# Optimization experiments

Measured on AMD Instinct MI355X. Metric: run time of the kernel, lower is better.

## Reference

```python
import jax, jax.numpy as jnp
import numpy as np

N_NODES = 30000
N_EDGES = 300000
NUM_GRAPHS = 512
HID = 600
IN_FEATS = 9
NUM_TASKS = 128


def setup_inputs() -> dict:
    key = jax.random.key(0)
    ks = jax.random.split(key, 20)
    s = 0.05  # small init scale to keep activations bounded over 5 layers
    inp = {
        'x': jax.random.normal(ks[0], (N_NODES, IN_FEATS), jnp.float32),
        'edge_index': jax.random.randint(ks[1], (2, N_EDGES), 0, N_NODES, jnp.int64),
        'batch_ind': jnp.sort(jax.random.randint(ks[2], (N_NODES,), 0, NUM_GRAPHS, jnp.int64)),
        'w1_0': jax.random.normal(ks[3], (IN_FEATS, HID), jnp.float32) * s,
        'b1_0': jax.random.normal(ks[4], (HID,), jnp.float32) * s,
        'w2_0': jax.random.normal(ks[5], (HID, HID), jnp.float32) * s,
        'b2_0': jax.random.normal(ks[6], (HID,), jnp.float32) * s,
        'w1_r': jax.random.normal(ks[7], (4, HID, HID), jnp.float32) * s,
        'b1_r': jax.random.normal(ks[8], (4, HID), jnp.float32) * s,
        'w2_r': jax.random.normal(ks[9], (4, HID, HID), jnp.float32) * s,
        'b2_r': jax.random.normal(ks[10], (4, HID), jnp.float32) * s,
        'cw1': jax.random.normal(ks[11], (HID, 256), jnp.float32) * s,
        'cb1': jax.random.normal(ks[12], (256,), jnp.float32) * s,
        'cw2': jax.random.normal(ks[13], (256, 256), jnp.float32) * s,
        'cb2': jax.random.normal(ks[14], (256,), jnp.float32) * s,
        'cw3': jax.random.normal(ks[15], (256, NUM_TASKS), jnp.float32) * s,
        'cb3': jax.random.normal(ks[16], (NUM_TASKS,), jnp.float32) * s,
    }
    return inp


def _gin_conv(h, edge_index, w1, b1, w2, b2):
    # sum-aggregate neighbor features: messages flow src -> dst
    msgs = h[edge_index[0]]                                   # [E, d] gather
    agg = jax.ops.segment_sum(msgs, edge_index[1], num_segments=N_NODES)
    z = h + agg                                               # (1 + eps) * x + agg, eps = 0
    z = jax.nn.relu(z @ w1 + b1) @ w2 + b2                    # per-layer MLP [in, 600, 600]
    return z


def _forward(x, edge_index, batch_ind, w1_0, b1_0, w2_0, b2_0,
             w1_r, b1_r, w2_r, b2_r, cw1, cb1, cw2, cb2, cw3, cb3):
    h = _gin_conv(x, edge_index, w1_0, b1_0, w2_0, b2_0)
    h = jax.nn.relu(h)  # inter-layer activation (dropout is identity in eval)
    for i in range(4):  # layers 1..4 (fixed, structurally distinct params)
        h = _gin_conv(h, edge_index, w1_r[i], b1_r[i], w2_r[i], b2_r[i])
        if i < 3:
            h = jax.nn.relu(h)  # no act/dropout after final GNN layer (jk=None)
    feats = jax.ops.segment_sum(h, batch_ind, num_segments=NUM_GRAPHS)  # global_add_pool
    z = jax.nn.relu(feats @ cw1 + cb1)
    z = jax.nn.relu(z @ cw2 + cb2)
    return z @ cw3 + cb3  # [NUM_GRAPHS, NUM_TASKS]


def reference(x, edge_index, batch_ind, w1_0, b1_0, w2_0, b2_0,
              w1_r, b1_r, w2_r, b2_r, cw1, cb1, cw2, cb2, cw3, cb3):
    return _forward(x, edge_index, batch_ind, w1_0, b1_0, w2_0, b2_0,
                    w1_r, b1_r, w2_r, b2_r, cw1, cb1, cw2, cb2, cw3, cb3)
```

## Files before the change

### kernel.cpp

```cpp
#include <hip/hip_runtime.h>

#define N_NODES 30000
#define N_EDGES 300000
#define NUM_GRAPHS 512
#define HID 600
#define IN_FEATS 9
#define NUM_TASKS 128

#define MPAD 30080
#define HPAD 640
#define K0PAD 32

typedef __attribute__((ext_vector_type(4))) float f32x4;
typedef __attribute__((ext_vector_type(8))) short bf16x8;


__device__ __forceinline__ float bflo(unsigned int v) {
  union { unsigned int u; float f; } c; c.u = v << 16; return c.f;
}
__device__ __forceinline__ float bfhi(unsigned int v) {
  union { unsigned int u; float f; } c; c.u = v & 0xffff0000u; return c.f;
}
__device__ __forceinline__ unsigned short f2bf(float f) {
  union { float f; unsigned int u; } c; c.f = f;
  unsigned int u = c.u;
  return (unsigned short)((u + 0x7fffu + ((u >> 16) & 1u)) >> 16);
}
__device__ __forceinline__ unsigned int pack2(float a, float b) {
  return (unsigned int)f2bf(a) | ((unsigned int)f2bf(b) << 16);
}


__global__ void k_hist(const int* __restrict__ keys, int* __restrict__ counts, int n) {
  int i = blockIdx.x * blockDim.x + threadIdx.x;
  if (i < n) atomicAdd(&counts[keys[i]], 1);
}

__global__ __launch_bounds__(1024) void k_exscan(const int* __restrict__ in,
                                                 int* __restrict__ out,
                                                 int* cursor, int n) {
  __shared__ int buf[1024];
  int tid = threadIdx.x;
  int CH = (n + 1023) / 1024;
  int base = tid * CH;
  int s = 0;
  for (int j = 0; j < CH; ++j) {
    int i = base + j;
    if (i < n) s += in[i];
  }
  buf[tid] = s;
  __syncthreads();
  for (int off = 1; off < 1024; off <<= 1) {
    int t = (tid >= off) ? buf[tid - off] : 0;
    __syncthreads();
    buf[tid] += t;
    __syncthreads();
  }
  int pre = (tid == 0) ? 0 : buf[tid - 1];
  for (int j = 0; j < CH; ++j) {
    int i = base + j;
    if (i <= n) out[i] = pre;
    if (i < n) {
      int v = in[i];
      if (cursor) cursor[i] = pre;
      pre += v;
    }
  }
}

__global__ __launch_bounds__(256) void k_scan1(const int* __restrict__ in,
                                               int* __restrict__ partials, int n) {
  __shared__ int buf[256];
  int i = blockIdx.x * 256 + threadIdx.x;
  buf[threadIdx.x] = (i < n) ? in[i] : 0;
  __syncthreads();
  for (int off = 128; off; off >>= 1) {
    if (threadIdx.x < off) buf[threadIdx.x] += buf[threadIdx.x + off];
    __syncthreads();
  }
  if (threadIdx.x == 0) partials[blockIdx.x] = buf[0];
}

__global__ __launch_bounds__(256) void k_scan3(const int* __restrict__ in,
                                               const int* __restrict__ poff,
                                               int* __restrict__ out,
                                               int* __restrict__ cursor, int n) {
  __shared__ int buf[256];
  int b = blockIdx.x, t = threadIdx.x;
  int i = b * 256 + t;
  int v = (i < n) ? in[i] : 0;
  buf[t] = v;
  __syncthreads();
  for (int off = 1; off < 256; off <<= 1) {
    int x = (t >= off) ? buf[t - off] : 0;
    __syncthreads();
    buf[t] += x;
    __syncthreads();
  }
  int base = poff[b];
  int excl = base + buf[t] - v;
  if (i < n) {
    out[i] = excl;
    cursor[i] = excl;
    if (i == n - 1) out[n] = base + buf[t];
  }
}

__global__ void k_scatter(const int* __restrict__ src, const int* __restrict__ dst,
                          int* __restrict__ cursor, int* __restrict__ edge_src, int E) {
  int e = blockIdx.x * blockDim.x + threadIdx.x;
  if (e < E) {
    int pos = atomicAdd(&cursor[dst[e]], 1);
    edge_src[pos] = src[e];
  }
}


__global__ void k_wt0(const float* __restrict__ w1_0, unsigned short* __restrict__ wt0) {
  int idx = blockIdx.x * 256 + threadIdx.x;
  if (idx >= HPAD * K0PAD) return;
  int n = idx / K0PAD, k = idx % K0PAD;
  float v = (n < HID && k < IN_FEATS) ? w1_0[(size_t)k * HID + n] : 0.f;
  wt0[idx] = f2bf(v);
}

__global__ __launch_bounds__(256) void k_wt_tiled(
    const float* __restrict__ w2_0, const float* __restrict__ w1_r,
    const float* __restrict__ w2_r, unsigned short* __restrict__ wts) {
  __shared__ float tile[64][65];
  int b = blockIdx.x;
  int w = b / 100;
  int tb = b % 100;
  int tn = (tb % 10) * 64;
  int tk = (tb / 10) * 64;
  const float* W;
  if (w == 0) W = w2_0;
  else if (w < 5) W = w1_r + (size_t)(w - 1) * HID * HID;
  else W = w2_r + (size_t)(w - 5) * HID * HID;
  int t = threadIdx.x;
  int lx = t & 63, ly = t >> 6;
#pragma unroll
  for (int i = 0; i < 16; ++i) {
    int k = tk + ly + i * 4;
    int n = tn + lx;
    float v = (k < HID && n < HID) ? W[(size_t)k * HID + n] : 0.f;
    tile[ly + i * 4][lx] = v;
  }
  __syncthreads();
  unsigned short* dst = wts + (size_t)w * HPAD * HPAD;
#pragma unroll
  for (int i = 0; i < 16; ++i) {
    int n = tn + ly + i * 4;
    int k = tk + lx;
    dst[(size_t)n * HPAD + k] = f2bf(tile[lx][ly + i * 4]);
  }
}

__global__ void k_bias_all(const float* __restrict__ b1_0, const float* __restrict__ b2_0,
                           const float* __restrict__ b1_r, const float* __restrict__ b2_r,
                           float* __restrict__ biases) {
  int idx = blockIdx.x * 256 + threadIdx.x;
  if (idx >= 10 * HPAD) return;
  int w = idx / HPAD, i = idx % HPAD;
  float v = 0.f;
  if (i < HID) {
    if (w == 0) v = b1_0[i];
    else if (w == 1) v = b2_0[i];
    else if (w < 6) v = b1_r[(size_t)(w - 2) * HID + i];
    else v = b2_r[(size_t)(w - 6) * HID + i];
  }
  biases[idx] = v;
}

__global__ void k_xconv(const float* __restrict__ x, unsigned short* __restrict__ xb) {
  int idx = blockIdx.x * 256 + threadIdx.x;
  if (idx >= MPAD * K0PAD) return;
  int m = idx >> 5, k = idx & 31;
  float v = (m < N_NODES && k < IN_FEATS) ? x[(size_t)m * IN_FEATS + k] : 0.f;
  xb[idx] = f2bf(v);
}


template <int U>
__global__ __launch_bounds__(256) void k_agg_bf16(
    const unsigned int* __restrict__ h, const int* __restrict__ ptr,
    const int* __restrict__ esrc, unsigned int* __restrict__ z, int n_nodes) {
  int wave = threadIdx.x >> 6, lane = threadIdx.x & 63;
  int node = blockIdx.x * 4 + wave;
  if (node >= n_nodes) return;
  int beg = ptr[node], end = ptr[node + 1];
  const unsigned int* hn = h + (size_t)node * U;
  float a0[5], a1[5];
#pragma unroll
  for (int i = 0; i < 5; ++i) {
    int u = lane + i * 64;
    if (u < U) { unsigned int v = hn[u]; a0[i] = bflo(v); a1[i] = bfhi(v); }
    else { a0[i] = 0.f; a1[i] = 0.f; }
  }
  int e = beg;
  for (; e + 4 <= end; e += 4) {
    const unsigned int* p0 = h + (size_t)esrc[e] * U;
    const unsigned int* p1 = h + (size_t)esrc[e + 1] * U;
    const unsigned int* p2 = h + (size_t)esrc[e + 2] * U;
    const unsigned int* p3 = h + (size_t)esrc[e + 3] * U;
    unsigned int v0[5], v1[5], v2[5], v3[5];
#pragma unroll
    for (int i = 0; i < 5; ++i) {
      int u = lane + i * 64;
      if (u < U) { v0[i] = p0[u]; v1[i] = p1[u]; v2[i] = p2[u]; v3[i] = p3[u]; }
      else { v0[i] = 0; v1[i] = 0; v2[i] = 0; v3[i] = 0; }
    }
#pragma unroll
    for (int i = 0; i < 5; ++i) {
      a0[i] += (bflo(v0[i]) + bflo(v1[i])) + (bflo(v2[i]) + bflo(v3[i]));
      a1[i] += (bfhi(v0[i]) + bfhi(v1[i])) + (bfhi(v2[i]) + bfhi(v3[i]));
    }
  }
  for (; e < end; ++e) {
    const unsigned int* p0 = h + (size_t)esrc[e] * U;
#pragma unroll
    for (int i = 0; i < 5; ++i) {
      int u = lane + i * 64;
      if (u < U) { unsigned int v = p0[u]; a0[i] += bflo(v); a1[i] += bfhi(v); }
    }
  }
  unsigned int* zn = z + (size_t)node * U;
#pragma unroll
  for (int i = 0; i < 5; ++i) {
    int u = lane + i * 64;
    if (u < U) zn[u] = pack2(a0[i], a1[i]);
  }
}


__global__ __launch_bounds__(256) void k_pool_bf16(
    const unsigned int* __restrict__ h, const int* __restrict__ gptr,
    float* __restrict__ feats) {
  const int U = HPAD / 2;
  __shared__ float red[4][HPAD];
  int t = threadIdx.x;
  int wave = t >> 6, lane = t & 63;
  int g = blockIdx.x;
  int beg = gptr[g], end = gptr[g + 1];
  float a0[5] = {0.f, 0.f, 0.f, 0.f, 0.f}, a1[5] = {0.f, 0.f, 0.f, 0.f, 0.f};
  for (int i = beg + wave; i < end; i += 4) {
    const unsigned int* hi = h + (size_t)i * U;
#pragma unroll
    for (int j = 0; j < 5; ++j) {
      unsigned int v = hi[lane + j * 64];
      a0[j] += bflo(v); a1[j] += bfhi(v);
    }
  }
#pragma unroll
  for (int j = 0; j < 5; ++j) {
    int u = lane + j * 64;
    red[wave][2 * u] = a0[j];
    red[wave][2 * u + 1] = a1[j];
  }
  __syncthreads();
  float* fg = feats + (size_t)g * HPAD;
  for (int c = t; c < HPAD; c += 256)
    fg[c] = red[0][c] + red[1][c] + red[2][c] + red[3][c];
}


#define GLOAD(gptr, lptr)                                                            \
  __builtin_amdgcn_global_load_lds(                                                  \
      (const __attribute__((address_space(1))) unsigned int*)(gptr),                 \
      (__attribute__((address_space(3))) unsigned int*)(lptr), 16, 0, 0)

__global__ __launch_bounds__(512, 6) void k_mgemm(
    const unsigned short* __restrict__ A, const unsigned short* __restrict__ Bt,
    const float* __restrict__ bias, unsigned short* __restrict__ C,
    int lda, int ldb, int ldc, int K, int relu, int gy) {
  int G = gridDim.x;
  int orig = blockIdx.x;
  int q = G >> 3, r = G & 7;
  int xcd = orig & 7, local = orig >> 3;
  int wgid = (xcd < r ? xcd * (q + 1) : r * (q + 1) + (xcd - r) * q) + local;
  int n0 = (wgid % gy) * 128;
  int m0 = (wgid / gy) * 128;

  __shared__ unsigned short smem[3 * 4096 * 2];
  unsigned short* Asb = smem;
  unsigned short* Bsb = smem + 12288;

  int t = threadIdx.x;
  int lane = t & 63, wave = t >> 6;
  int wm = (wave >> 2) * 64;
  int wn = (wave & 3) * 32;

  f32x4 acc[4][2] = {};

  int off = t * 8;
  int rm = off >> 5, rk = off & 31;

  const unsigned short* Ar = A + (size_t)(m0 + rm) * lda + rk;
  const unsigned short* Br = Bt + (size_t)(n0 + rm) * ldb + rk;

  int nt = K >> 5;
  GLOAD(Ar, Asb + off);
  GLOAD(Br, Bsb + off);
  if (nt > 1) {
    GLOAD(Ar + 32, Asb + 4096 + off);
    GLOAD(Br + 32, Bsb + 4096 + off);
  }

  int kk = (lane >> 4) * 8;
  int ra = wm + (lane & 15);
  int rb = wn + (lane & 15);
  int cur = 0;

  for (int tt = 0; tt < nt; ++tt) {
    if (tt + 1 < nt) {
      asm volatile("s_waitcnt vmcnt(2)" ::: "memory");
    } else {
      asm volatile("s_waitcnt vmcnt(0)" ::: "memory");
    }
    __builtin_amdgcn_s_barrier();
    if (tt + 2 < nt) {
      int k2 = (tt + 2) << 5;
      int nb = cur + 2; if (nb >= 3) nb -= 3;
      GLOAD(Ar + k2, Asb + nb * 4096 + off);
      GLOAD(Br + k2, Bsb + nb * 4096 + off);
    }
    bf16x8 a[4], b[2];
#pragma unroll
    for (int i = 0; i < 4; ++i)
      a[i] = *(const bf16x8*)(Asb + cur * 4096 + (ra + i * 16) * 32 + kk);
#pragma unroll
    for (int j = 0; j < 2; ++j)
      b[j] = *(const bf16x8*)(Bsb + cur * 4096 + (rb + j * 16) * 32 + kk);
#pragma unroll
    for (int i = 0; i < 4; ++i)
#pragma unroll
      for (int j = 0; j < 2; ++j)
        acc[i][j] = __builtin_amdgcn_mfma_f32_16x16x32_bf16(b[j], a[i], acc[i][j], 0, 0, 0);
    cur += 1; if (cur >= 3) cur = 0;
  }

  __syncthreads();
  int colm = lane & 15;
  int nq = (lane >> 4) * 4;
#pragma unroll
  for (int j = 0; j < 2; ++j) {
    int nloc = wn + j * 16 + nq;
    f32x4 bv = *(const f32x4*)&bias[n0 + nloc];
#pragma unroll
    for (int i = 0; i < 4; ++i) {
      int mloc = wm + i * 16 + colm;
      float v0 = acc[i][j][0] + bv[0];
      float v1 = acc[i][j][1] + bv[1];
      float v2 = acc[i][j][2] + bv[2];
      float v3 = acc[i][j][3] + bv[3];
      if (relu) {
        v0 = fmaxf(v0, 0.f); v1 = fmaxf(v1, 0.f);
        v2 = fmaxf(v2, 0.f); v3 = fmaxf(v3, 0.f);
      }
      uint2 w;
      w.x = pack2(v0, v1);
      w.y = pack2(v2, v3);
      int nblk = (nloc >> 2) ^ ((mloc & 7) << 2);
      *(uint2*)&smem[mloc * 128 + nblk * 4] = w;
    }
  }
  __syncthreads();
#pragma unroll
  for (int p = 0; p < 4; ++p) {
    int idx = p * 4096 + t * 8;
    int mloc = idx >> 7;
    int ncol = idx & 127;
    int s = (mloc & 7) << 2;
    int nb0 = (ncol >> 2) ^ s;
    int nb1 = ((ncol >> 2) + 1) ^ s;
    uint2 w0 = *(uint2*)&smem[mloc * 128 + nb0 * 4];
    uint2 w1 = *(uint2*)&smem[mloc * 128 + nb1 * 4];
    uint4 w;
    w.x = w0.x; w.y = w0.y; w.z = w1.x; w.w = w1.y;
    *(uint4*)&C[(size_t)(m0 + mloc) * ldc + n0 + ncol] = w;
  }
}


__global__ __launch_bounds__(256) void k_classifier(
    const float* __restrict__ feats,
    const float* __restrict__ cw1, const float* __restrict__ cb1,
    const float* __restrict__ cw2, const float* __restrict__ cb2,
    const float* __restrict__ cw3, const float* __restrict__ cb3,
    float* __restrict__ out) {
  __shared__ float f[HID];
  __shared__ float red[4][256];
  __shared__ float z1[256];
  __shared__ float z2[256];
  int g = blockIdx.x;
  int t = threadIdx.x;
  int wave = t >> 6, lane = t & 63;
  for (int i = t; i < HID; i += 256) f[i] = feats[(size_t)g * HPAD + i];
  __syncthreads();

  {
    float acc[4] = {0.f, 0.f, 0.f, 0.f};
    int k0 = wave * 150, k1 = k0 + 150;
    for (int k = k0; k < k1; ++k) {
      float fv = f[k];
      const float* row = cw1 + (size_t)k * 256;
#pragma unroll
      for (int j = 0; j < 4; ++j) acc[j] += fv * row[lane + j * 64];
    }
#pragma unroll
    for (int j = 0; j < 4; ++j) red[wave][lane + j * 64] = acc[j];
  }
  __syncthreads();
  z1[t] = fmaxf(red[0][t] + red[1][t] + red[2][t] + red[3][t] + cb1[t], 0.f);
  __syncthreads();

  {
    float acc[4] = {0.f, 0.f, 0.f, 0.f};
    int k0 = wave * 64, k1 = k0 + 64;
    for (int k = k0; k < k1; ++k) {
      float zv = z1[k];
      const float* row = cw2 + (size_t)k * 256;
#pragma unroll
      for (int j = 0; j < 4; ++j) acc[j] += zv * row[lane + j * 64];
    }
    __syncthreads();
#pragma unroll
    for (int j = 0; j < 4; ++j) red[wave][lane + j * 64] = acc[j];
  }
  __syncthreads();
  z2[t] = fmaxf(red[0][t] + red[1][t] + red[2][t] + red[3][t] + cb2[t], 0.f);
  __syncthreads();

  {
    float a0 = 0.f, a1 = 0.f;
    int k0 = wave * 64, k1 = k0 + 64;
    for (int k = k0; k < k1; ++k) {
      float zv = z2[k];
      const float* row = cw3 + (size_t)k * NUM_TASKS;
      a0 += zv * row[lane];
      a1 += zv * row[lane + 64];
    }
    __syncthreads();
    red[wave][lane] = a0;
    red[wave][lane + 64] = a1;
  }
  __syncthreads();
  if (t < NUM_TASKS)
    out[(size_t)g * NUM_TASKS + t] = red[0][t] + red[1][t] + red[2][t] + red[3][t] + cb3[t];
}


extern "C" void kernel_launch(void* const* d_in, const int* in_sizes, int n_in,
                              void* d_out, int out_size, void* d_ws, size_t ws_size,
                              hipStream_t stream) {
  const float* x      = (const float*)d_in[0];
  const int*   ei     = (const int*)d_in[1];
  const int*   batch  = (const int*)d_in[2];
  const float* w1_0   = (const float*)d_in[3];
  const float* b1_0   = (const float*)d_in[4];
  const float* w2_0   = (const float*)d_in[5];
  const float* b2_0   = (const float*)d_in[6];
  const float* w1_r   = (const float*)d_in[7];
  const float* b1_r   = (const float*)d_in[8];
  const float* w2_r   = (const float*)d_in[9];
  const float* b2_r   = (const float*)d_in[10];
  const float* cw1    = (const float*)d_in[11];
  const float* cb1    = (const float*)d_in[12];
  const float* cw2    = (const float*)d_in[13];
  const float* cb2    = (const float*)d_in[14];
  const float* cw3    = (const float*)d_in[15];
  const float* cb3    = (const float*)d_in[16];
  float* out = (float*)d_out;

  const int* e_src = ei;
  const int* e_dst = ei + N_EDGES;

  const size_t HBUF = (size_t)MPAD * HPAD;
  const size_t ZBUF = (size_t)MPAD * K0PAD;
  const size_t WT   = (size_t)HPAD * HPAD;
  const int NB = (N_NODES + 255) / 256;

  unsigned short* hA  = (unsigned short*)d_ws;
  unsigned short* hB  = hA + HBUF;
  unsigned short* hC  = hB + HBUF;
  unsigned short* z0  = hC + HBUF;
  unsigned short* xb  = z0 + ZBUF;
  unsigned short* wt0 = xb + ZBUF;
  unsigned short* wts = wt0 + (size_t)HPAD * K0PAD;
  float* biases = (float*)(wts + 9 * WT);
  float* feats  = biases + 10 * HPAD;
  int* row_ptr  = (int*)(feats + (size_t)NUM_GRAPHS * HPAD);
  int* counts   = row_ptr + (N_NODES + 1);
  int* edge_src = counts + N_NODES;
  int* gptr     = edge_src + N_EDGES;
  int* gcnt     = gptr + (NUM_GRAPHS + 1);
  int* partials = gcnt + NUM_GRAPHS;
  int* poff     = partials + (NB + 1);

  k_wt0<<<(HPAD * K0PAD + 255) / 256, 256, 0, stream>>>(w1_0, wt0);
  k_wt_tiled<<<9 * 100, 256, 0, stream>>>(w2_0, w1_r, w2_r, wts);
  k_bias_all<<<(10 * HPAD + 255) / 256, 256, 0, stream>>>(b1_0, b2_0, b1_r, b2_r, biases);
  k_xconv<<<(MPAD * K0PAD + 255) / 256, 256, 0, stream>>>(x, xb);

  hipMemsetAsync(counts, 0, N_NODES * sizeof(int), stream);
  k_hist<<<(N_EDGES + 255) / 256, 256, 0, stream>>>(e_dst, counts, N_EDGES);
  k_scan1<<<NB, 256, 0, stream>>>(counts, partials, N_NODES);
  k_exscan<<<1, 1024, 0, stream>>>(partials, poff, nullptr, NB);
  k_scan3<<<NB, 256, 0, stream>>>(counts, poff, row_ptr, counts, N_NODES);
  k_scatter<<<(N_EDGES + 255) / 256, 256, 0, stream>>>(e_src, e_dst, counts, edge_src, N_EDGES);

  hipMemsetAsync(gcnt, 0, NUM_GRAPHS * sizeof(int), stream);
  k_hist<<<(N_NODES + 255) / 256, 256, 0, stream>>>(batch, gcnt, N_NODES);
  k_exscan<<<1, 1024, 0, stream>>>(gcnt, gptr, nullptr, NUM_GRAPHS);

  const int G = (MPAD / 128) * (HPAD / 128);
  const int GY = HPAD / 128;

  k_agg_bf16<K0PAD / 2><<<(N_NODES + 3) / 4, 256, 0, stream>>>(
      (const unsigned int*)xb, row_ptr, edge_src, (unsigned int*)z0, N_NODES);
  k_mgemm<<<G, 512, 0, stream>>>(z0, wt0, biases + 0 * HPAD, hC, K0PAD, K0PAD, HPAD, K0PAD, 1, GY);
  k_mgemm<<<G, 512, 0, stream>>>(hC, wts, biases + 1 * HPAD, hA, HPAD, HPAD, HPAD, HPAD, 1, GY);

  unsigned short* h = hA;
  unsigned short* z = hB;
  unsigned short* tb = hC;
  for (int i = 0; i < 4; ++i) {
    k_agg_bf16<HPAD / 2><<<(N_NODES + 3) / 4, 256, 0, stream>>>(
        (const unsigned int*)h, row_ptr, edge_src, (unsigned int*)z, N_NODES);
    k_mgemm<<<G, 512, 0, stream>>>(z, wts + (1 + (size_t)i) * WT, biases + (2 + i) * HPAD, tb,
                                   HPAD, HPAD, HPAD, HPAD, 1, GY);
    k_mgemm<<<G, 512, 0, stream>>>(tb, wts + (5 + (size_t)i) * WT, biases + (6 + i) * HPAD, z,
                                   HPAD, HPAD, HPAD, HPAD, (i < 3) ? 1 : 0, GY);
    unsigned short* tmp = h; h = z; z = tmp;
  }

  k_pool_bf16<<<NUM_GRAPHS, 256, 0, stream>>>((const unsigned int*)h, gptr, feats);
  k_classifier<<<NUM_GRAPHS, 256, 0, stream>>>(feats, cw1, cb1, cw2, cb2, cw3, cb3, out);
}
```

Before: 720.9 us.

## Add 256x128 32x32-MFMA GEMM for late layers and fuse pooling with classifier

Adds a new GEMM kernel with 256-row tiles that uses 32x32x16 bf16 MFMA instructions, a three-stage LDS buffer and direct global-to-LDS loads. It is used only for layers 3 and 4, while the earlier layers keep the 128x128 kernel. MPAD grows to a multiple of 256 so the larger tiles divide the rows evenly. Graph pooling and the classifier MLP are merged into one kernel, which removes a launch and the round trip of the feats buffer through global memory. The larger tile is meant to improve operand reuse, at the cost of more LDS and lower occupancy per CU, and the mixed kernel selection per layer looks experimental.

```diff
diff --git a/kernel.cpp b/kernel.cpp
--- a/kernel.cpp
+++ b/kernel.cpp
@@ -7,11 +7,12 @@
 #define IN_FEATS 9
 #define NUM_TASKS 128
 
-#define MPAD 30080
+#define MPAD 30208
 #define HPAD 640
 #define K0PAD 32
 
 typedef __attribute__((ext_vector_type(4))) float f32x4;
+typedef __attribute__((ext_vector_type(16))) float f32x16;
 typedef __attribute__((ext_vector_type(8))) short bf16x8;
 
 
@@ -233,37 +234,6 @@
 }
 
 
-__global__ __launch_bounds__(256) void k_pool_bf16(
-    const unsigned int* __restrict__ h, const int* __restrict__ gptr,
-    float* __restrict__ feats) {
-  const int U = HPAD / 2;
-  __shared__ float red[4][HPAD];
-  int t = threadIdx.x;
-  int wave = t >> 6, lane = t & 63;
-  int g = blockIdx.x;
-  int beg = gptr[g], end = gptr[g + 1];
-  float a0[5] = {0.f, 0.f, 0.f, 0.f, 0.f}, a1[5] = {0.f, 0.f, 0.f, 0.f, 0.f};
-  for (int i = beg + wave; i < end; i += 4) {
-    const unsigned int* hi = h + (size_t)i * U;
-#pragma unroll
-    for (int j = 0; j < 5; ++j) {
-      unsigned int v = hi[lane + j * 64];
-      a0[j] += bflo(v); a1[j] += bfhi(v);
-    }
-  }
-#pragma unroll
-  for (int j = 0; j < 5; ++j) {
-    int u = lane + j * 64;
-    red[wave][2 * u] = a0[j];
-    red[wave][2 * u + 1] = a1[j];
-  }
-  __syncthreads();
-  float* fg = feats + (size_t)g * HPAD;
-  for (int c = t; c < HPAD; c += 256)
-    fg[c] = red[0][c] + red[1][c] + red[2][c] + red[3][c];
-}
-
-
 #define GLOAD(gptr, lptr)                                                            \
   __builtin_amdgcn_global_load_lds(                                                  \
       (const __attribute__((address_space(1))) unsigned int*)(gptr),                 \
@@ -382,20 +352,164 @@
 }
 
 
-__global__ __launch_bounds__(256) void k_classifier(
-    const float* __restrict__ feats,
+__global__ __launch_bounds__(512, 4) void k_mgemm32(
+    const unsigned short* __restrict__ A, const unsigned short* __restrict__ Bt,
+    const float* __restrict__ bias, unsigned short* __restrict__ C,
+    int lda, int ldb, int ldc, int K, int relu, int gy) {
+  int G = gridDim.x;
+  int orig = blockIdx.x;
+  int q = G >> 3, r = G & 7;
+  int xcd = orig & 7, local = orig >> 3;
+  int wgid = (xcd < r ? xcd * (q + 1) : r * (q + 1) + (xcd - r) * q) + local;
+  int n0 = (wgid % gy) * 128;
+  int m0 = (wgid / gy) * 256;
+
+  __shared__ unsigned short smem[36864];
+  unsigned short* Asb = smem;
+  unsigned short* Bsb = smem + 24576;
+
+  int t = threadIdx.x;
+  int lane = t & 63, wave = t >> 6;
+  int wm = (wave >> 1) * 64;
+  int wn = (wave & 1) * 64;
+
+  f32x16 acc[2][2] = {};
+
+  int offc = t * 8;
+  int rmc = offc >> 5, rkc = offc & 31;
+  const unsigned short* ArA0 = A + (size_t)(m0 + rmc) * lda + rkc;
+  const unsigned short* ArA1 = A + (size_t)(m0 + 128 + rmc) * lda + rkc;
+  const unsigned short* ArB  = Bt + (size_t)(n0 + rmc) * ldb + rkc;
+
+  int nt = K >> 5;
+
+#define STAGE32(buf, koff)                                  \
+  do {                                                      \
+    GLOAD(ArA0 + (koff), Asb + (buf) * 8192 + offc);        \
+    GLOAD(ArA1 + (koff), Asb + (buf) * 8192 + 4096 + offc); \
+    GLOAD(ArB + (koff), Bsb + (buf) * 4096 + offc);         \
+  } while (0)
+
+  STAGE32(0, 0);
+  if (nt > 1) STAGE32(1, 32);
+
+  int r32 = lane & 31, half = lane >> 5;
+  int koff = half * 8;
+  int cur = 0;
+
+  for (int tt = 0; tt < nt; ++tt) {
+    if (tt + 1 < nt) {
+      asm volatile("s_waitcnt vmcnt(3)" ::: "memory");
+    } else {
+      asm volatile("s_waitcnt vmcnt(0)" ::: "memory");
+    }
+    __builtin_amdgcn_s_barrier();
+    if (tt + 2 < nt) {
+      int nb = cur + 2; if (nb >= 3) nb -= 3;
+      STAGE32(nb, (tt + 2) << 5);
+    }
+    const unsigned short* Ab = Asb + cur * 8192;
+    const unsigned short* Bb = Bsb + cur * 4096;
+#pragma unroll
+    for (int ks = 0; ks < 2; ++ks) {
+      bf16x8 a[2], b[2];
+#pragma unroll
+      for (int i = 0; i < 2; ++i)
+        a[i] = *(const bf16x8*)(Ab + (wm + i * 32 + r32) * 32 + ks * 16 + koff);
+#pragma unroll
+      for (int j = 0; j < 2; ++j)
+        b[j] = *(const bf16x8*)(Bb + (wn + j * 32 + r32) * 32 + ks * 16 + koff);
+#pragma unroll
+      for (int i = 0; i < 2; ++i)
+#pragma unroll
+        for (int j = 0; j < 2; ++j)
+          acc[i][j] = __builtin_amdgcn_mfma_f32_32x32x16_bf16(b[j], a[i], acc[i][j], 0, 0, 0);
+    }
+    cur += 1; if (cur >= 3) cur = 0;
+  }
+
+  __syncthreads();
+#pragma unroll
+  for (int fm = 0; fm < 2; ++fm) {
+    int mloc = wm + fm * 32 + r32;
+#pragma unroll
+    for (int fn = 0; fn < 2; ++fn) {
+#pragma unroll
+      for (int rg = 0; rg < 4; ++rg) {
+        int nbase = wn + fn * 32 + rg * 8 + 4 * half;
+        f32x4 bv = *(const f32x4*)&bias[n0 + nbase];
+        float v0 = acc[fm][fn][rg * 4 + 0] + bv[0];
+        float v1 = acc[fm][fn][rg * 4 + 1] + bv[1];
+        float v2 = acc[fm][fn][rg * 4 + 2] + bv[2];
+        float v3 = acc[fm][fn][rg * 4 + 3] + bv[3];
+        if (relu) {
+          v0 = fmaxf(v0, 0.f); v1 = fmaxf(v1, 0.f);
+          v2 = fmaxf(v2, 0.f); v3 = fmaxf(v3, 0.f);
+        }
+        uint2 w;
+        w.x = pack2(v0, v1);
+        w.y = pack2(v2, v3);
+        int nblk = (nbase >> 2) ^ ((mloc & 7) << 2);
+        *(uint2*)&smem[mloc * 128 + nblk * 4] = w;
+      }
+    }
+  }
+  __syncthreads();
+#pragma unroll
+  for (int p = 0; p < 8; ++p) {
+    int idx = p * 4096 + t * 8;
+    int mloc = idx >> 7;
+    int ncol = idx & 127;
+    int s = (mloc & 7) << 2;
+    int nb0 = (ncol >> 2) ^ s;
+    int nb1 = ((ncol >> 2) + 1) ^ s;
+    uint2 w0 = *(uint2*)&smem[mloc * 128 + nb0 * 4];
+    uint2 w1 = *(uint2*)&smem[mloc * 128 + nb1 * 4];
+    uint4 w;
+    w.x = w0.x; w.y = w0.y; w.z = w1.x; w.w = w1.y;
+    *(uint4*)&C[(size_t)(m0 + mloc) * ldc + n0 + ncol] = w;
+  }
+#undef STAGE32
+}
+
+
+__global__ __launch_bounds__(256) void k_poolcls(
+    const unsigned int* __restrict__ h, const int* __restrict__ gptr,
     const float* __restrict__ cw1, const float* __restrict__ cb1,
     const float* __restrict__ cw2, const float* __restrict__ cb2,
     const float* __restrict__ cw3, const float* __restrict__ cb3,
     float* __restrict__ out) {
-  __shared__ float f[HID];
-  __shared__ float red[4][256];
+  const int U = HPAD / 2;
+  __shared__ float red[4][HPAD];
+  __shared__ float f[HPAD];
+  __shared__ float red2[4][256];
   __shared__ float z1[256];
   __shared__ float z2[256];
   int g = blockIdx.x;
   int t = threadIdx.x;
   int wave = t >> 6, lane = t & 63;
-  for (int i = t; i < HID; i += 256) f[i] = feats[(size_t)g * HPAD + i];
+  int beg = gptr[g], end = gptr[g + 1];
+
+  {
+    float a0[5] = {0.f, 0.f, 0.f, 0.f, 0.f}, a1[5] = {0.f, 0.f, 0.f, 0.f, 0.f};
+    for (int i = beg + wave; i < end; i += 4) {
+      const unsigned int* hi = h + (size_t)i * U;
+#pragma unroll
+      for (int j = 0; j < 5; ++j) {
+        unsigned int v = hi[lane + j * 64];
+        a0[j] += bflo(v); a1[j] += bfhi(v);
+      }
+    }
+#pragma unroll
+    for (int j = 0; j < 5; ++j) {
+      int u = lane + j * 64;
+      red[wave][2 * u] = a0[j];
+      red[wave][2 * u + 1] = a1[j];
+    }
+  }
+  __syncthreads();
+  for (int c = t; c < HPAD; c += 256)
+    f[c] = red[0][c] + red[1][c] + red[2][c] + red[3][c];
   __syncthreads();
 
   {
@@ -408,10 +522,10 @@
       for (int j = 0; j < 4; ++j) acc[j] += fv * row[lane + j * 64];
     }
 #pragma unroll
-    for (int j = 0; j < 4; ++j) red[wave][lane + j * 64] = acc[j];
-  }
-  __syncthreads();
-  z1[t] = fmaxf(red[0][t] + red[1][t] + red[2][t] + red[3][t] + cb1[t], 0.f);
+    for (int j = 0; j < 4; ++j) red2[wave][lane + j * 64] = acc[j];
+  }
+  __syncthreads();
+  z1[t] = fmaxf(red2[0][t] + red2[1][t] + red2[2][t] + red2[3][t] + cb1[t], 0.f);
   __syncthreads();
 
   {
@@ -425,10 +539,10 @@
     }
     __syncthreads();
 #pragma unroll
-    for (int j = 0; j < 4; ++j) red[wave][lane + j * 64] = acc[j];
-  }
-  __syncthreads();
-  z2[t] = fmaxf(red[0][t] + red[1][t] + red[2][t] + red[3][t] + cb2[t], 0.f);
+    for (int j = 0; j < 4; ++j) red2[wave][lane + j * 64] = acc[j];
+  }
+  __syncthreads();
+  z2[t] = fmaxf(red2[0][t] + red2[1][t] + red2[2][t] + red2[3][t] + cb2[t], 0.f);
   __syncthreads();
 
   {
@@ -441,12 +555,12 @@
       a1 += zv * row[lane + 64];
     }
     __syncthreads();
-    red[wave][lane] = a0;
-    red[wave][lane + 64] = a1;
+    red2[wave][lane] = a0;
+    red2[wave][lane + 64] = a1;
   }
   __syncthreads();
   if (t < NUM_TASKS)
-    out[(size_t)g * NUM_TASKS + t] = red[0][t] + red[1][t] + red[2][t] + red[3][t] + cb3[t];
+    out[(size_t)g * NUM_TASKS + t] = red2[0][t] + red2[1][t] + red2[2][t] + red2[3][t] + cb3[t];
 }
 
 
@@ -488,8 +602,7 @@
   unsigned short* wt0 = xb + ZBUF;
   unsigned short* wts = wt0 + (size_t)HPAD * K0PAD;
   float* biases = (float*)(wts + 9 * WT);
-  float* feats  = biases + 10 * HPAD;
-  int* row_ptr  = (int*)(feats + (size_t)NUM_GRAPHS * HPAD);
+  int* row_ptr  = (int*)(biases + 10 * HPAD);
   int* counts   = row_ptr + (N_NODES + 1);
   int* edge_src = counts + N_NODES;
   int* gptr     = edge_src + N_EDGES;
@@ -513,13 +626,14 @@
   k_hist<<<(N_NODES + 255) / 256, 256, 0, stream>>>(batch, gcnt, N_NODES);
   k_exscan<<<1, 1024, 0, stream>>>(gcnt, gptr, nullptr, NUM_GRAPHS);
 
-  const int G = (MPAD / 128) * (HPAD / 128);
+  const int G16 = (MPAD / 128) * (HPAD / 128);
+  const int G32 = (MPAD / 256) * (HPAD / 128);
   const int GY = HPAD / 128;
 
   k_agg_bf16<K0PAD / 2><<<(N_NODES + 3) / 4, 256, 0, stream>>>(
       (const unsigned int*)xb, row_ptr, edge_src, (unsigned int*)z0, N_NODES);
-  k_mgemm<<<G, 512, 0, stream>>>(z0, wt0, biases + 0 * HPAD, hC, K0PAD, K0PAD, HPAD, K0PAD, 1, GY);
-  k_mgemm<<<G, 512, 0, stream>>>(hC, wts, biases + 1 * HPAD, hA, HPAD, HPAD, HPAD, HPAD, 1, GY);
+  k_mgemm<<<G16, 512, 0, stream>>>(z0, wt0, biases + 0 * HPAD, hC, K0PAD, K0PAD, HPAD, K0PAD, 1, GY);
+  k_mgemm<<<G16, 512, 0, stream>>>(hC, wts, biases + 1 * HPAD, hA, HPAD, HPAD, HPAD, HPAD, 1, GY);
 
   unsigned short* h = hA;
   unsigned short* z = hB;
@@ -527,13 +641,20 @@
   for (int i = 0; i < 4; ++i) {
     k_agg_bf16<HPAD / 2><<<(N_NODES + 3) / 4, 256, 0, stream>>>(
         (const unsigned int*)h, row_ptr, edge_src, (unsigned int*)z, N_NODES);
-    k_mgemm<<<G, 512, 0, stream>>>(z, wts + (1 + (size_t)i) * WT, biases + (2 + i) * HPAD, tb,
-                                   HPAD, HPAD, HPAD, HPAD, 1, GY);
-    k_mgemm<<<G, 512, 0, stream>>>(tb, wts + (5 + (size_t)i) * WT, biases + (6 + i) * HPAD, z,
-                                   HPAD, HPAD, HPAD, HPAD, (i < 3) ? 1 : 0, GY);
+    if (i < 2) {
+      k_mgemm<<<G16, 512, 0, stream>>>(z, wts + (1 + (size_t)i) * WT, biases + (2 + i) * HPAD, tb,
+                                       HPAD, HPAD, HPAD, HPAD, 1, GY);
+      k_mgemm<<<G16, 512, 0, stream>>>(tb, wts + (5 + (size_t)i) * WT, biases + (6 + i) * HPAD, z,
+                                       HPAD, HPAD, HPAD, HPAD, 1, GY);
+    } else {
+      k_mgemm32<<<G32, 512, 0, stream>>>(z, wts + (1 + (size_t)i) * WT, biases + (2 + i) * HPAD, tb,
+                                         HPAD, HPAD, HPAD, HPAD, 1, GY);
+      k_mgemm32<<<G32, 512, 0, stream>>>(tb, wts + (5 + (size_t)i) * WT, biases + (6 + i) * HPAD, z,
+                                         HPAD, HPAD, HPAD, HPAD, (i < 3) ? 1 : 0, GY);
+    }
     unsigned short* tmp = h; h = z; z = tmp;
   }
 
-  k_pool_bf16<<<NUM_GRAPHS, 256, 0, stream>>>((const unsigned int*)h, gptr, feats);
-  k_classifier<<<NUM_GRAPHS, 256, 0, stream>>>(feats, cw1, cb1, cw2, cb2, cw3, cb3, out);
-}
+  k_poolcls<<<NUM_GRAPHS, 256, 0, stream>>>((const unsigned int*)h, gptr,
+                                            cw1, cb1, cw2, cb2, cw3, cb3, out);
+}
```

After: 761.5 us. 1.06x slower.
